# Performance work log

Hardware: AMD Instinct MI355X
Metric: run time of the kernel (lower is better)

The kernel has to match this reference:

```python
import jax, jax.numpy as jnp
import numpy as np

N = 2048          # segment length (init arg)
NFFT = 4096       # 2**ceil(log2(2*N-1))
BATCH = 64
NSEG = 128        # number of overlap-add segments per example


def setup_inputs() -> dict:
    key = jax.random.key(0)
    k1, k2, k3, k4, k5, k6 = jax.random.split(key, 6)
    x = jax.random.normal(k1, (BATCH, NSEG * N), dtype=jnp.float32)
    # learned scalar params (torch init: g=0, R=0, m_*=1; small jitter for non-trivial grads)
    g = 0.1 * jax.random.normal(k2, (1,), dtype=jnp.float32)
    R = 0.1 * jax.random.normal(k3, (1,), dtype=jnp.float32)
    m_hp = jnp.ones((1,), jnp.float32) + 0.1 * jax.random.normal(k4, (1,), dtype=jnp.float32)
    m_bp = jnp.ones((1,), jnp.float32) + 0.1 * jax.random.normal(k5, (1,), dtype=jnp.float32)
    m_lp = jnp.ones((1,), jnp.float32) + 0.1 * jax.random.normal(k6, (1,), dtype=jnp.float32)
    return {"x": x, "g": g, "R": R, "m_hp": m_hp, "m_bp": m_bp, "m_lp": m_lp}


def reference(x, g, R, m_hp, m_bp, m_lp):
    # SVF coefficient mapping
    gt = jnp.tan(jnp.pi * jax.nn.sigmoid(g) / 2)      # (1,)
    Rt = jax.nn.softplus(R)                            # (1,)
    g2 = gt * gt
    b = jnp.concatenate([g2 * m_lp + gt * m_bp + m_hp,
                         2 * g2 * m_lp - 2 * m_hp,
                         g2 * m_lp - gt * m_bp + m_hp])  # (3,)
    a = jnp.concatenate([g2 + 2 * Rt * gt + 1,
                         2 * g2 - 2,
                         g2 - 2 * Rt * gt + 1])          # (3,)

    # FFT overlap-add filtering (training path)
    segs = x.reshape(x.shape[0], -1, N)                # [B, S, N]
    X = jnp.fft.rfft(segs, n=NFFT, axis=-1)            # [B, S, NFFT//2+1] complex
    H = jnp.fft.rfft(b, n=NFFT) / jnp.fft.rfft(a, n=NFFT)
    y = jnp.fft.irfft(X * H, n=NFFT, axis=-1)          # [B, S, NFFT]

    first = y[..., :N]                                 # [B, S, N]
    overlap = y[:, :-1, N:2 * N]                       # [B, S-1, N]
    overlap_ext = jnp.pad(overlap, ((0, 0), (1, 0), (0, 0)))  # shift right by one segment
    return (first + overlap_ext).reshape(x.shape[0], -1)
```

## Files before the change

### kernel.cpp

```cpp
#include <hip/hip_runtime.h>
#include <math.h>


#define N_PER_ROW (128 * 2048)
#define BATCH 64
#define TPB 256
#define OUT_BLK 32
#define WARM 64
#define TILE (TPB * OUT_BLK)
#define TILES_PER_ROW (N_PER_ROW / TILE)
#define LDS_LOGICAL (TILE + WARM)
#define LDS_FLOATS (LDS_LOGICAL + (LDS_LOGICAL / 32) + 4)

__device__ __forceinline__ int padidx(int L) { return L + (L >> 5); }

__global__ __launch_bounds__(256, 4) void dsvf_iir_kernel(
    const float* __restrict__ x,
    const float* __restrict__ g_p, const float* __restrict__ R_p,
    const float* __restrict__ mhp_p, const float* __restrict__ mbp_p,
    const float* __restrict__ mlp_p,
    float* __restrict__ out)
{
    __shared__ float lds[LDS_FLOATS];

    const int b   = blockIdx.x;
    const int row = b >> 5;
    const int tl  = b & (TILES_PER_ROW - 1);
    const size_t base = (size_t)row * N_PER_ROW + (size_t)tl * TILE;
    const float* __restrict__ src = x + base;
    const int k = threadIdx.x;

    if (k < WARM / 4) {
        float4 v;
        if (tl == 0) { v.x = v.y = v.z = v.w = 0.0f; }
        else         { v = *((const float4*)(src - WARM) + k); }
        float* p = &lds[padidx(4 * k)];
        p[0] = v.x; p[1] = v.y; p[2] = v.z; p[3] = v.w;
    }
    {
        const float4* sp = (const float4*)src;
        #pragma unroll
        for (int m = 0; m < TILE / 4 / TPB; ++m) {
            const int i = k + m * TPB;
            float4 v = sp[i];
            float* p = &lds[padidx(WARM + 4 * i)];
            p[0] = v.x; p[1] = v.y; p[2] = v.z; p[3] = v.w;
        }
    }

    const float g = g_p[0], R = R_p[0];
    const float m_hp = mhp_p[0], m_bp = mbp_p[0], m_lp = mlp_p[0];
    const float sig = 1.0f / (1.0f + expf(-g));
    const float gt  = tanf(1.5707963267948966f * sig);
    const float Rt  = log1pf(expf(R));
    const float g2  = gt * gt;
    const float b0 = g2 * m_lp + gt * m_bp + m_hp;
    const float b1 = 2.0f * g2 * m_lp - 2.0f * m_hp;
    const float b2 = g2 * m_lp - gt * m_bp + m_hp;
    const float a0 = g2 + 2.0f * Rt * gt + 1.0f;
    const float a1 = 2.0f * g2 - 2.0f;
    const float a2 = g2 - 2.0f * Rt * gt + 1.0f;
    const float inv_a0 = 1.0f / a0;
    const float B0 = b0 * inv_a0, B1 = b1 * inv_a0, B2 = b2 * inv_a0;
    const float A1 = a1 * inv_a0, A2 = a2 * inv_a0;

    __syncthreads();

    float s1 = 0.0f, s2 = 0.0f;
    const int L0 = k * OUT_BLK;

#define STEP_D(xx) { float y_ = fmaf(B0, (xx), s1);                 \
                     s1 = fmaf(-A1, y_, fmaf(B1, (xx), s2));        \
                     s2 = fmaf(-A2, y_, B2 * (xx)); }
#define STEP_S(xx, yy) { (yy) = fmaf(B0, (xx), s1);                 \
                     s1 = fmaf(-A1, (yy), fmaf(B1, (xx), s2));      \
                     s2 = fmaf(-A2, (yy), B2 * (xx)); }

    #pragma unroll
    for (int j = 0; j < WARM / 4; ++j) {
        const float* p = &lds[padidx(L0 + 4 * j)];
        STEP_D(p[0]); STEP_D(p[1]); STEP_D(p[2]); STEP_D(p[3]);
    }

    float o[OUT_BLK];
    #pragma unroll
    for (int j = 0; j < OUT_BLK / 4; ++j) {
        const float* p = &lds[padidx(L0 + WARM + 4 * j)];
        STEP_S(p[0], o[4*j+0]); STEP_S(p[1], o[4*j+1]);
        STEP_S(p[2], o[4*j+2]); STEP_S(p[3], o[4*j+3]);
    }
#undef STEP_D
#undef STEP_S

    __syncthreads();

    #pragma unroll
    for (int j = 0; j < OUT_BLK; ++j) {
        lds[padidx(L0 + j)] = o[j];
    }

    __syncthreads();

    {
        float4* dp = (float4*)(out + base);
        #pragma unroll
        for (int m = 0; m < TILE / 4 / TPB; ++m) {
            const int i = k + m * TPB;
            const float* p = &lds[padidx(4 * i)];
            float4 v;
            v.x = p[0]; v.y = p[1]; v.z = p[2]; v.w = p[3];
            dp[i] = v;
        }
    }
}

extern "C" void kernel_launch(void* const* d_in, const int* in_sizes, int n_in,
                              void* d_out, int out_size, void* d_ws, size_t ws_size,
                              hipStream_t stream) {
    const float* x    = (const float*)d_in[0];
    const float* g    = (const float*)d_in[1];
    const float* R    = (const float*)d_in[2];
    const float* m_hp = (const float*)d_in[3];
    const float* m_bp = (const float*)d_in[4];
    const float* m_lp = (const float*)d_in[5];
    float* out = (float*)d_out;

    dim3 block(TPB);
    dim3 grid(BATCH * TILES_PER_ROW);
    dsvf_iir_kernel<<<grid, block, 0, stream>>>(x, g, R, m_hp, m_bp, m_lp, out);
}
```

Before: 120.7 us.

## Replace serial IIR warmup with precomputed impulse-response dot product, halve per-thread block

The 64-sample serial warm-up recurrence is replaced by a dot product against precomputed state-response coefficients (computed once per block into LDS), which breaks the dependency chain into two independent FMA accumulators. Threads per block double to 512 and outputs per thread halve to 16, which shortens the serial chain per thread and raises parallelism. The trade-off is more warm-up work relative to useful output per thread, a serial coefficient loop (up to 64 steps) in the first 64 threads before the barrier, and summation order changes that slightly alter floating-point rounding.

```diff
diff --git a/kernel.cpp b/kernel.cpp
--- a/kernel.cpp
+++ b/kernel.cpp
@@ -4,8 +4,8 @@
 
 #define N_PER_ROW (128 * 2048)
 #define BATCH 64
-#define TPB 256
-#define OUT_BLK 32
+#define TPB 512
+#define OUT_BLK 16
 #define WARM 64
 #define TILE (TPB * OUT_BLK)
 #define TILES_PER_ROW (N_PER_ROW / TILE)
@@ -14,7 +14,7 @@
 
 __device__ __forceinline__ int padidx(int L) { return L + (L >> 5); }
 
-__global__ __launch_bounds__(256, 4) void dsvf_iir_kernel(
+__global__ __launch_bounds__(TPB, 8) void dsvf_iir_kernel(
     const float* __restrict__ x,
     const float* __restrict__ g_p, const float* __restrict__ R_p,
     const float* __restrict__ mhp_p, const float* __restrict__ mbp_p,
@@ -22,6 +22,8 @@
     float* __restrict__ out)
 {
     __shared__ float lds[LDS_FLOATS];
+    __shared__ float c1s[WARM];
+    __shared__ float c2s[WARM];
 
     const int b   = blockIdx.x;
     const int row = b >> 5;
@@ -64,24 +66,34 @@
     const float B0 = b0 * inv_a0, B1 = b1 * inv_a0, B2 = b2 * inv_a0;
     const float A1 = a1 * inv_a0, A2 = a2 * inv_a0;
 
+    if (k < WARM) {
+        float w1 = fmaf(-A1, B0, B1);
+        float w2 = fmaf(-A2, B0, B2);
+        for (int i = 0; i < k; ++i) {
+            float t1 = fmaf(-A1, w1, w2);
+            float t2 = -A2 * w1;
+            w1 = t1; w2 = t2;
+        }
+        c1s[WARM - 1 - k] = w1;
+        c2s[WARM - 1 - k] = w2;
+    }
+
     __syncthreads();
 
-    float s1 = 0.0f, s2 = 0.0f;
     const int L0 = k * OUT_BLK;
+    float s1a = 0.0f, s2a = 0.0f, s1b = 0.0f, s2b = 0.0f;
+    #pragma unroll
+    for (int j = 0; j < WARM; j += 2) {
+        const float xa = lds[padidx(L0 + j)];
+        const float xb = lds[padidx(L0 + j + 1)];
+        s1a = fmaf(c1s[j],     xa, s1a);  s2a = fmaf(c2s[j],     xa, s2a);
+        s1b = fmaf(c1s[j + 1], xb, s1b);  s2b = fmaf(c2s[j + 1], xb, s2b);
+    }
+    float s1 = s1a + s1b, s2 = s2a + s2b;
 
-#define STEP_D(xx) { float y_ = fmaf(B0, (xx), s1);                 \
-                     s1 = fmaf(-A1, y_, fmaf(B1, (xx), s2));        \
-                     s2 = fmaf(-A2, y_, B2 * (xx)); }
 #define STEP_S(xx, yy) { (yy) = fmaf(B0, (xx), s1);                 \
                      s1 = fmaf(-A1, (yy), fmaf(B1, (xx), s2));      \
                      s2 = fmaf(-A2, (yy), B2 * (xx)); }
-
-    #pragma unroll
-    for (int j = 0; j < WARM / 4; ++j) {
-        const float* p = &lds[padidx(L0 + 4 * j)];
-        STEP_D(p[0]); STEP_D(p[1]); STEP_D(p[2]); STEP_D(p[3]);
-    }
-
     float o[OUT_BLK];
     #pragma unroll
     for (int j = 0; j < OUT_BLK / 4; ++j) {
@@ -89,7 +101,6 @@
         STEP_S(p[0], o[4*j+0]); STEP_S(p[1], o[4*j+1]);
         STEP_S(p[2], o[4*j+2]); STEP_S(p[3], o[4*j+3]);
     }
-#undef STEP_D
 #undef STEP_S
 
     __syncthreads();
```

After: 122.2 us. Within noise of the previous version (+1.2%).

## Use swizzled float4 LDS layout and halve IIR warm-up length

Applied to the files above, without the earlier changes.

Replaces the padded scalar LDS layout with a float4 array indexed through an XOR swizzle, so every shared-memory read and write becomes a 128-bit access while staying free of bank conflicts. This cuts the number of LDS instructions for staging, the recurrence, and writeback. The warm-up prefix that primes each thread's IIR state also drops from 64 to 32 samples, which removes serial recurrence steps. The shorter warm-up could raise approximation error at tile boundaries if the filter's impulse response decays slowly.

```diff
diff --git a/kernel.cpp b/kernel.cpp
--- a/kernel.cpp
+++ b/kernel.cpp
@@ -6,22 +6,23 @@
 #define BATCH 64
 #define TPB 256
 #define OUT_BLK 32
-#define WARM 64
+#define WARM 32
 #define TILE (TPB * OUT_BLK)
 #define TILES_PER_ROW (N_PER_ROW / TILE)
-#define LDS_LOGICAL (TILE + WARM)
-#define LDS_FLOATS (LDS_LOGICAL + (LDS_LOGICAL / 32) + 4)
+#define LDS_F4 ((TILE + WARM) / 4)
 
-__device__ __forceinline__ int padidx(int L) { return L + (L >> 5); }
+__device__ __forceinline__ int sw(int I) {
+    return (I & ~7) | ((I ^ (I >> 3)) & 7);
+}
 
-__global__ __launch_bounds__(256, 4) void dsvf_iir_kernel(
+__global__ __launch_bounds__(TPB, 4) void dsvf_iir_kernel(
     const float* __restrict__ x,
     const float* __restrict__ g_p, const float* __restrict__ R_p,
     const float* __restrict__ mhp_p, const float* __restrict__ mbp_p,
     const float* __restrict__ mlp_p,
     float* __restrict__ out)
 {
-    __shared__ float lds[LDS_FLOATS];
+    __shared__ float4 lds4[LDS_F4];
 
     const int b   = blockIdx.x;
     const int row = b >> 5;
@@ -33,18 +34,15 @@
     if (k < WARM / 4) {
         float4 v;
         if (tl == 0) { v.x = v.y = v.z = v.w = 0.0f; }
-        else         { v = *((const float4*)(src - WARM) + k); }
-        float* p = &lds[padidx(4 * k)];
-        p[0] = v.x; p[1] = v.y; p[2] = v.z; p[3] = v.w;
+        else         { v = *((const float4*)src - WARM / 4 + k); }
+        lds4[sw(k)] = v;
     }
     {
         const float4* sp = (const float4*)src;
         #pragma unroll
         for (int m = 0; m < TILE / 4 / TPB; ++m) {
             const int i = k + m * TPB;
-            float4 v = sp[i];
-            float* p = &lds[padidx(WARM + 4 * i)];
-            p[0] = v.x; p[1] = v.y; p[2] = v.z; p[3] = v.w;
+            lds4[sw(WARM / 4 + i)] = sp[i];
         }
     }
 
@@ -67,7 +65,7 @@
     __syncthreads();
 
     float s1 = 0.0f, s2 = 0.0f;
-    const int L0 = k * OUT_BLK;
+    const int I0 = k * (OUT_BLK / 4);
 
 #define STEP_D(xx) { float y_ = fmaf(B0, (xx), s1);                 \
                      s1 = fmaf(-A1, y_, fmaf(B1, (xx), s2));        \
@@ -78,16 +76,16 @@
 
     #pragma unroll
     for (int j = 0; j < WARM / 4; ++j) {
-        const float* p = &lds[padidx(L0 + 4 * j)];
-        STEP_D(p[0]); STEP_D(p[1]); STEP_D(p[2]); STEP_D(p[3]);
+        float4 v = lds4[sw(I0 + j)];
+        STEP_D(v.x); STEP_D(v.y); STEP_D(v.z); STEP_D(v.w);
     }
 
-    float o[OUT_BLK];
+    float4 o[OUT_BLK / 4];
     #pragma unroll
     for (int j = 0; j < OUT_BLK / 4; ++j) {
-        const float* p = &lds[padidx(L0 + WARM + 4 * j)];
-        STEP_S(p[0], o[4*j+0]); STEP_S(p[1], o[4*j+1]);
-        STEP_S(p[2], o[4*j+2]); STEP_S(p[3], o[4*j+3]);
+        float4 v = lds4[sw(I0 + WARM / 4 + j)];
+        STEP_S(v.x, o[j].x); STEP_S(v.y, o[j].y);
+        STEP_S(v.z, o[j].z); STEP_S(v.w, o[j].w);
     }
 #undef STEP_D
 #undef STEP_S
@@ -95,8 +93,8 @@
     __syncthreads();
 
     #pragma unroll
-    for (int j = 0; j < OUT_BLK; ++j) {
-        lds[padidx(L0 + j)] = o[j];
+    for (int j = 0; j < OUT_BLK / 4; ++j) {
+        lds4[sw(I0 + j)] = o[j];
     }
 
     __syncthreads();
@@ -106,10 +104,7 @@
         #pragma unroll
         for (int m = 0; m < TILE / 4 / TPB; ++m) {
             const int i = k + m * TPB;
-            const float* p = &lds[padidx(4 * i)];
-            float4 v;
-            v.x = p[0]; v.y = p[1]; v.z = p[2]; v.w = p[3];
-            dp[i] = v;
+            dp[i] = lds4[sw(i)];
         }
     }
 }
```

Result: no change. 121.3 us (+0.5%).
